# Optimization experiments

Hardware: AMD Instinct MI355X
Metric: run time of the kernel (lower is better)

Reference implementation:

```python
import jax, jax.numpy as jnp
import numpy as np

TIME = 4096
DIM = 2048
DT_TAU = 0.1 / 1.0  # dt / tau


def setup_inputs() -> dict:
    key = jax.random.key(0)
    k1, k2, k3, k4 = jax.random.split(key, 4)
    inputs = jax.random.normal(k1, (TIME, 1, DIM), dtype=jnp.float32)
    W = jax.random.normal(k2, (DIM, DIM), dtype=jnp.float32) * 0.02  # recurrent weight (nn.Linear, bias=False)
    bias = jax.random.normal(k3, (1, DIM), dtype=jnp.float32)
    initial = jax.random.normal(k4, (1, DIM), dtype=jnp.float32)
    return {"inputs": inputs, "W": W, "bias": bias, "initial": initial}


def reference(inputs, W, bias, initial):
    # states[0] = initial; states[t+1] = s*(1-dt/tau) + (dt/tau)*(sigmoid(s+bias)@W.T + inputs[t])
    def step(state, x_t):
        f = jax.nn.sigmoid(state + bias) @ W.T  # [1, dim]
        new_state = state * (1.0 - DT_TAU) + DT_TAU * (f + x_t)
        return new_state, new_state

    _, rest = jax.lax.scan(step, initial, inputs[: TIME - 1])  # rest: [time-1, 1, dim]
    return jnp.concatenate([initial[None], rest], axis=0)  # [time, 1, dim]
```

## Files before the change

kernel.cpp:

```cpp
#include <hip/hip_runtime.h>
#include <hip/hip_fp16.h>
#include <hip/hip_cooperative_groups.h>
#include <stdint.h>

#define TIME_STEPS 4096
#define DIM        2048
#define NBLK       256
#define NTH        512
#define NWORK      32
#define WVB        8
#define RPW        8

typedef uint32_t u32x4 __attribute__((ext_vector_type(4)));
typedef _Float16 h2f16 __attribute__((ext_vector_type(2)));


__device__ __forceinline__ uint32_t umin32(uint32_t a, uint32_t b) { return a < b ? a : b; }

__device__ __forceinline__ float dot2f(uint32_t packed, h2f16 w, float acc) {
#if __has_builtin(__builtin_amdgcn_fdot2)
  return __builtin_amdgcn_fdot2(__builtin_bit_cast(h2f16, packed), w, acc, false);
#else
  h2f16 a = __builtin_bit_cast(h2f16, packed);
  acc = fmaf((float)a.x, (float)w.x, acc);
  return fmaf((float)a.y, (float)w.y, acc);
#endif
}

__device__ __forceinline__ int swz(int p) { return p ^ (((p >> 5) & 7) << 2); }

template<int NSLOT>
__global__ __launch_bounds__(NTH, 2) void ctrnn_kernel(
    const float* __restrict__ x,
    const float* __restrict__ W,
    const float* __restrict__ bias,
    const float* __restrict__ initial,
    float* __restrict__ out,
    uint32_t* __restrict__ actbuf,
    uint32_t* __restrict__ progress,
    uint32_t* __restrict__ xccmap)
{
  const int tid  = threadIdx.x;
  const int lane = tid & 63;
  const int wv   = tid >> 6;

  if (tid == 0) {
    uint32_t xcc;
    asm volatile("s_getreg_b32 %0, hwreg(HW_REG_XCC_ID)" : "=s"(xcc));
    __hip_atomic_store(&xccmap[blockIdx.x], xcc,
                       __ATOMIC_RELAXED, __HIP_MEMORY_SCOPE_AGENT);
  }
  cooperative_groups::this_grid().sync();

  __shared__ uint32_t s_map[NBLK];
  for (int i = tid; i < NBLK; i += NTH)
    s_map[i] = __hip_atomic_load(&xccmap[i], __ATOMIC_RELAXED, __HIP_MEMORY_SCOPE_AGENT);
  __syncthreads();
  const uint32_t target = s_map[0];
  int before = 0, total = 0, beforeN = 0;
  const int bid = blockIdx.x;
  for (int i = 0; i < NBLK; ++i) {
    const bool m = (s_map[i] == target);
    total += m;
    if (i < bid) { before += m; beforeN += !m; }
  }
  const bool mine = (s_map[bid] == target);
  const int rank = mine ? before : (total + beforeN);
  if (rank >= NWORK) return;
  const int wb = rank;

  __shared__ uint32_t lds[2][1024];

  const int gwid = wb * WVB + wv;
  const int row0 = gwid * RPW;

  h2f16 w2[RPW][16];
  #pragma unroll
  for (int m = 0; m < RPW; ++m) {
    const float* wr = W + (size_t)(row0 + m) * DIM + lane * 32;
    #pragma unroll
    for (int q = 0; q < 16; ++q)
      w2[m][q] = h2f16{(_Float16)wr[2*q], (_Float16)wr[2*q+1]};
  }

  float v = 0.f, bj = 0.f, xv = 0.f, xw = 0.f;
  if (lane < RPW) {
    const int j = row0 + lane;
    v  = initial[j];
    bj = bias[j];
    xv = x[j];
    xw = x[DIM + j];
    out[j] = v;
    const float a0 = 1.0f / (1.0f + __expf(-(v + bj)));
    __half h = __float2half_rn(a0);
    uint16_t hb; __builtin_memcpy(&hb, &h, 2);
    __hip_atomic_store(&actbuf[j], (1u << 16) | hb,
                       __ATOMIC_RELAXED, __HIP_MEMORY_SCOPE_AGENT);
  }

  const int e0 = wv * 256 + lane * 4;
  const int p0 = e0 >> 1;

  uint32_t prog_seen = 0;

  for (int t = 0; t < TIME_STEPS - 1; ++t) {
    const int b = t & 1;
    const uint32_t needtag = (uint32_t)(t + 1);
    const uint32_t thresh  = needtag << 16;

    const uint32_t* qsrc = actbuf + (size_t)(t & (NSLOT - 1)) * DIM + e0;
    u32x4 q;
    for (;;) {
      asm volatile("global_load_dwordx4 %0, %1, off sc1\n\t"
                   "s_waitcnt vmcnt(0)"
                   : "=v"(q) : "v"(qsrc) : "memory");
      const uint32_t mn = umin32(umin32(q[0], q[1]), umin32(q[2], q[3]));
      if (mn >= thresh) break;
      __builtin_amdgcn_s_sleep(1);
    }

    {
      const uint32_t lo = __builtin_amdgcn_perm(q[1], q[0], 0x05040100u);
      const uint32_t hi = __builtin_amdgcn_perm(q[3], q[2], 0x05040100u);
      const int w0 = swz(p0);
      lds[b][w0]     = lo;
      lds[b][w0 + 1] = hi;
    }

    __syncthreads();

    if (tid == 0)
      __hip_atomic_store(&progress[wb], needtag,
                         __ATOMIC_RELAXED, __HIP_MEMORY_SCOPE_AGENT);

    float xn = 0.f;
    if (lane < RPW && t + 2 < TIME_STEPS) xn = x[(size_t)(t + 2) * DIM + row0 + lane];

    float a0 = 0.f, a1 = 0.f, a2 = 0.f, a3 = 0.f;
    float a4 = 0.f, a5 = 0.f, a6 = 0.f, a7 = 0.f;
    #pragma unroll
    for (int j = 0; j < 4; ++j) {
      const u32x4 qq = *reinterpret_cast<const u32x4*>(&lds[b][swz(lane * 16 + 4 * j)]);
      #pragma unroll
      for (int i = 0; i < 4; ++i) {
        const uint32_t pr = qq[i];
        const int idx = 4 * j + i;
        a0 = dot2f(pr, w2[0][idx], a0);
        a1 = dot2f(pr, w2[1][idx], a1);
        a2 = dot2f(pr, w2[2][idx], a2);
        a3 = dot2f(pr, w2[3][idx], a3);
        a4 = dot2f(pr, w2[4][idx], a4);
        a5 = dot2f(pr, w2[5][idx], a5);
        a6 = dot2f(pr, w2[6][idx], a6);
        a7 = dot2f(pr, w2[7][idx], a7);
      }
    }

    const float t0 = a0 + __shfl_xor(a0, 1, 64);
    const float t1 = a1 + __shfl_xor(a1, 1, 64);
    const float t2 = a2 + __shfl_xor(a2, 1, 64);
    const float t3 = a3 + __shfl_xor(a3, 1, 64);
    const float t4 = a4 + __shfl_xor(a4, 1, 64);
    const float t5 = a5 + __shfl_xor(a5, 1, 64);
    const float t6 = a6 + __shfl_xor(a6, 1, 64);
    const float t7 = a7 + __shfl_xor(a7, 1, 64);
    float b0 = (lane & 1) ? t1 : t0;
    float b1 = (lane & 1) ? t3 : t2;
    float b2 = (lane & 1) ? t5 : t4;
    float b3 = (lane & 1) ? t7 : t6;
    b0 += __shfl_xor(b0, 2, 64);
    b1 += __shfl_xor(b1, 2, 64);
    b2 += __shfl_xor(b2, 2, 64);
    b3 += __shfl_xor(b3, 2, 64);
    float c0 = (lane & 2) ? b1 : b0;
    float c1 = (lane & 2) ? b3 : b2;
    c0 += __shfl_xor(c0, 4, 64);
    c1 += __shfl_xor(c1, 4, 64);
    float p = (lane & 4) ? c1 : c0;
    p += __shfl_xor(p, 8, 64);
    p += __shfl_xor(p, 16, 64);
    p += __shfl_xor(p, 32, 64);

    if (t >= NSLOT - 1) {
      const uint32_t need = (uint32_t)(t + 2 - NSLOT);
      if (need > prog_seen) {
        for (;;) {
          uint32_t mn = __hip_atomic_load(&progress[lane & (NWORK - 1)],
                            __ATOMIC_RELAXED, __HIP_MEMORY_SCOPE_AGENT);
          uint32_t qv;
          qv = (uint32_t)__shfl_xor((int)mn, 1, 64);  mn = umin32(mn, qv);
          qv = (uint32_t)__shfl_xor((int)mn, 2, 64);  mn = umin32(mn, qv);
          qv = (uint32_t)__shfl_xor((int)mn, 4, 64);  mn = umin32(mn, qv);
          qv = (uint32_t)__shfl_xor((int)mn, 8, 64);  mn = umin32(mn, qv);
          qv = (uint32_t)__shfl_xor((int)mn, 16, 64); mn = umin32(mn, qv);
          if (mn >= need) { prog_seen = mn; break; }
          __builtin_amdgcn_s_sleep(1);
        }
      }
    }

    if (lane < RPW) {
      v  = 0.9f * v + 0.1f * (p + xv);
      xv = xw;
      xw = xn;
      out[(size_t)(t + 1) * DIM + row0 + lane] = v;
      const float a = 1.0f / (1.0f + __expf(-(v + bj)));
      __half h = __float2half_rn(a);
      uint16_t hb; __builtin_memcpy(&hb, &h, 2);
      const uint32_t e = ((uint32_t)(t + 2) << 16) | hb;
      __hip_atomic_store(&actbuf[(size_t)((t + 1) & (NSLOT - 1)) * DIM + row0 + lane], e,
                         __ATOMIC_RELAXED, __HIP_MEMORY_SCOPE_AGENT);
    }
  }
}

extern "C" void kernel_launch(void* const* d_in, const int* in_sizes, int n_in,
                              void* d_out, int out_size, void* d_ws, size_t ws_size,
                              hipStream_t stream) {
  const float* x       = (const float*)d_in[0];
  const float* W       = (const float*)d_in[1];
  const float* bias    = (const float*)d_in[2];
  const float* initial = (const float*)d_in[3];
  float* out           = (float*)d_out;

  uint32_t* actbuf = (uint32_t*)d_ws;

  const size_t need8 = ((size_t)8 * DIM + NWORK + NBLK) * 4;
  void* kfun;
  size_t ringwords;
  if (ws_size >= need8) { kfun = (void*)ctrnn_kernel<8>; ringwords = (size_t)8 * DIM; }
  else                  { kfun = (void*)ctrnn_kernel<2>; ringwords = (size_t)2 * DIM; }

  uint32_t* progress = actbuf + ringwords;
  uint32_t* xccmap   = progress + NWORK;

  hipMemsetAsync(d_ws, 0, (ringwords + NWORK + NBLK) * 4, stream);

  void* args[] = { (void*)&x, (void*)&W, (void*)&bias, (void*)&initial,
                   (void*)&out, (void*)&actbuf, (void*)&progress, (void*)&xccmap };
  hipLaunchCooperativeKernel(kfun, dim3(NBLK), dim3(NTH), args, 0, stream);
}
```

Baseline: 9.321 ms.

## Batch input prefetch across 16 steps and restructure spin-wait polling

Input values for 16 timesteps are loaded at once across all 64 lanes, double-buffered, and picked per step with a cross-lane shuffle. This replaces a per-step global load by the 8 active lanes, taking that load off the latency-critical recurrence path. The spin-wait now repeats until every lane of the wave is satisfied, with no sleep between attempts. The activation broadcast store is moved ahead of the output store so the next step can start sooner. The cost is more register state and a busier polling loop.

```diff
diff --git a/kernel.cpp b/kernel.cpp
--- a/kernel.cpp
+++ b/kernel.cpp
@@ -83,13 +83,17 @@
       w2[m][q] = h2f16{(_Float16)wr[2*q], (_Float16)wr[2*q+1]};
   }
 
-  float v = 0.f, bj = 0.f, xv = 0.f, xw = 0.f;
+  const int xq = lane >> 3, xr = lane & 7;
+  float xa = x[(size_t)xq * DIM + row0 + xr];
+  float xb = x[(size_t)(8 + xq) * DIM + row0 + xr];
+  float xa2 = 0.f, xb2 = 0.f;
+  int t0 = 0;
+
+  float v = 0.f, bj = 0.f;
   if (lane < RPW) {
     const int j = row0 + lane;
     v  = initial[j];
     bj = bias[j];
-    xv = x[j];
-    xw = x[DIM + j];
     out[j] = v;
     const float a0 = 1.0f / (1.0f + __expf(-(v + bj)));
     __half h = __float2half_rn(a0);
@@ -105,19 +109,21 @@
 
   for (int t = 0; t < TIME_STEPS - 1; ++t) {
     const int b = t & 1;
+    const int off = t - t0;
     const uint32_t needtag = (uint32_t)(t + 1);
     const uint32_t thresh  = needtag << 16;
 
     const uint32_t* qsrc = actbuf + (size_t)(t & (NSLOT - 1)) * DIM + e0;
     u32x4 q;
-    for (;;) {
-      asm volatile("global_load_dwordx4 %0, %1, off sc1\n\t"
-                   "s_waitcnt vmcnt(0)"
-                   : "=v"(q) : "v"(qsrc) : "memory");
-      const uint32_t mn = umin32(umin32(q[0], q[1]), umin32(q[2], q[3]));
-      if (mn >= thresh) break;
-      __builtin_amdgcn_s_sleep(1);
-    }
+    bool ok = false;
+    do {
+      if (!ok) {
+        asm volatile("global_load_dwordx4 %0, %1, off sc1\n\t"
+                     "s_waitcnt vmcnt(0)"
+                     : "=&v"(q) : "v"(qsrc) : "memory");
+        ok = umin32(umin32(q[0], q[1]), umin32(q[2], q[3])) >= thresh;
+      }
+    } while (!__all((int)ok));
 
     {
       const uint32_t lo = __builtin_amdgcn_perm(q[1], q[0], 0x05040100u);
@@ -133,8 +139,12 @@
       __hip_atomic_store(&progress[wb], needtag,
                          __ATOMIC_RELAXED, __HIP_MEMORY_SCOPE_AGENT);
 
-    float xn = 0.f;
-    if (lane < RPW && t + 2 < TIME_STEPS) xn = x[(size_t)(t + 2) * DIM + row0 + lane];
+    if (off == 13) {
+      const int ta = min(t0 + 16 + xq, TIME_STEPS - 1);
+      const int tb = min(t0 + 24 + xq, TIME_STEPS - 1);
+      xa2 = x[(size_t)ta * DIM + row0 + xr];
+      xb2 = x[(size_t)tb * DIM + row0 + xr];
+    }
 
     float a0 = 0.f, a1 = 0.f, a2 = 0.f, a3 = 0.f;
     float a4 = 0.f, a5 = 0.f, a6 = 0.f, a7 = 0.f;
@@ -156,18 +166,18 @@
       }
     }
 
-    const float t0 = a0 + __shfl_xor(a0, 1, 64);
-    const float t1 = a1 + __shfl_xor(a1, 1, 64);
-    const float t2 = a2 + __shfl_xor(a2, 1, 64);
-    const float t3 = a3 + __shfl_xor(a3, 1, 64);
-    const float t4 = a4 + __shfl_xor(a4, 1, 64);
-    const float t5 = a5 + __shfl_xor(a5, 1, 64);
-    const float t6 = a6 + __shfl_xor(a6, 1, 64);
-    const float t7 = a7 + __shfl_xor(a7, 1, 64);
-    float b0 = (lane & 1) ? t1 : t0;
-    float b1 = (lane & 1) ? t3 : t2;
-    float b2 = (lane & 1) ? t5 : t4;
-    float b3 = (lane & 1) ? t7 : t6;
+    const float t0r = a0 + __shfl_xor(a0, 1, 64);
+    const float t1r = a1 + __shfl_xor(a1, 1, 64);
+    const float t2r = a2 + __shfl_xor(a2, 1, 64);
+    const float t3r = a3 + __shfl_xor(a3, 1, 64);
+    const float t4r = a4 + __shfl_xor(a4, 1, 64);
+    const float t5r = a5 + __shfl_xor(a5, 1, 64);
+    const float t6r = a6 + __shfl_xor(a6, 1, 64);
+    const float t7r = a7 + __shfl_xor(a7, 1, 64);
+    float b0 = (lane & 1) ? t1r : t0r;
+    float b1 = (lane & 1) ? t3r : t2r;
+    float b2 = (lane & 1) ? t5r : t4r;
+    float b3 = (lane & 1) ? t7r : t6r;
     b0 += __shfl_xor(b0, 2, 64);
     b1 += __shfl_xor(b1, 2, 64);
     b2 += __shfl_xor(b2, 2, 64);
@@ -199,18 +209,21 @@
       }
     }
 
+    const float xsrc = (off < 8) ? xa : xb;
+    const float xvt  = __shfl(xsrc, ((off & 7) << 3) | xr, 64);
+
     if (lane < RPW) {
-      v  = 0.9f * v + 0.1f * (p + xv);
-      xv = xw;
-      xw = xn;
-      out[(size_t)(t + 1) * DIM + row0 + lane] = v;
+      v = 0.9f * v + 0.1f * (p + xvt);
       const float a = 1.0f / (1.0f + __expf(-(v + bj)));
       __half h = __float2half_rn(a);
       uint16_t hb; __builtin_memcpy(&hb, &h, 2);
       const uint32_t e = ((uint32_t)(t + 2) << 16) | hb;
       __hip_atomic_store(&actbuf[(size_t)((t + 1) & (NSLOT - 1)) * DIM + row0 + lane], e,
                          __ATOMIC_RELAXED, __HIP_MEMORY_SCOPE_AGENT);
-    }
+      out[(size_t)(t + 1) * DIM + row0 + lane] = v;
+    }
+
+    if (off == 15) { t0 += 16; xa = xa2; xb = xb2; }
   }
 }
 
```

Result: slower. 9.568 ms (+2.6%).
